# Kernel optimization log

Hardware: AMD Instinct MI355X
Metric: run time of the kernel (lower is better)

The kernel has to match this reference:

```python
import jax, jax.numpy as jnp
import numpy as np

# GNB per-element parameters [s, beta, R, C6] indexed by atomic number Z (rows not listed stay zero)
_ROWS = {
 1:[0.2772,1.7504,3.6516,95.99], 2:[0.2425,2.087,2.1843,40.67], 3:[0.3266,2.3073,1.2711,70.21],
 4:[0.3964,2.8811,3.3497,114.51], 5:[0.3121,2.6366,2.7079,152.36], 6:[0.2455,3.0189,1.8219,184.28],
 7:[0.2743,2.9432,2.4667,482.54], 8:[0.2577,2.7407,2.365,405.57], 9:[0.2791,2.5863,1.5062,218.45],
 10:[0.2378,2.5307,1.8233,174.81], 11:[0.2592,2.5679,1.3974,181.7], 12:[0.3837,2.9613,3.3515,263.02],
 13:[0.3013,3.2377,3.0102,228.1], 14:[0.3202,3.2749,3.1629,359.43], 15:[0.3399,3.7491,3.2554,3222.12],
 16:[0.3215,3.6718,2.9539,2144.49], 17:[0.3071,3.418,3.0368,2072.46], 18:[0.2752,3.3306,2.6598,1357.42],
 19:[0.2264,2.9736,4.0877,1406.65], 20:[0.4015,3.4464,4.1275,1058.36], 21:[0.9388,4.5955,9.7282,11498.73],
 22:[0.6048,3.5334,8.5322,3361.33], 23:[0.3678,3.068,7.2344,2095.91], 24:[0.2848,2.8393,5.3605,1049.31],
 25:[0.355,3.055,3.718,966.27], 26:[0.4406,3.2628,3.6408,1571.36], 27:[0.4124,3.2622,3.4961,1183.59],
 28:[0.3139,2.749,3.5108,787.76], 29:[0.3345,2.9097,3.0537,563.93], 30:[0.3391,2.9024,3.0261,592.91],
 31:[0.3146,3.3924,3.1735,430.82], 32:[0.3327,3.2804,3.1773,812.57], 33:[0.404,3.8757,3.8357,4533.53],
 34:[0.3343,3.8562,3.1109,3440.92], 35:[0.3242,3.7067,3.2122,3859.82], 36:[0.292,3.6457,2.8263,2729.6],
 37:[0.2677,3.4421,2.412,1864.19], 38:[0.3446,3.559,1.894,1175.73], 39:[1.0038,5.7293,11.2061,32141.18],
 40:[0.6146,5.075,6.821,27655.14], 41:[0.4244,3.7156,7.2367,2864.2], 42:[0.4882,3.6853,3.901,3563.45],
 43:[0.4439,3.6987,4.0857,3266.43], 44:[0.4736,3.7826,4.045,3967.23], 45:[0.4039,3.4706,3.4813,2233.82],
 46:[0.3188,3.3433,3.0487,1393.49], 47:[0.2948,3.1186,2.7795,1315.09], 48:[0.3012,3.0853,2.8673,1311.47],
 49:[0.3351,3.5452,3.3339,1460.56], 50:[0.3134,3.2997,3.0086,1662.99], 51:[0.4081,4.1277,3.9919,8089.97],
 52:[0.3585,4.1795,3.4209,6887.05], 53:[0.3574,4.0988,3.5649,8799.32], 54:[0.3134,4.0387,3.0288,6136.5],
 55:[0.2872,3.8468,2.262,3757.31], 56:[0.3788,4.0368,1.3837,2561.18], 57:[1.0851,6.1365,12.171,66580.83],
 72:[0.5577,5.213,6.0791,27593.76], 73:[0.5308,4.7637,5.7661,15364.65], 74:[0.3926,3.6018,3.6366,2734.5],
 75:[0.5351,3.9552,4.241,4801.82], 76:[0.4701,4.0278,4.1348,5685.94], 77:[0.3661,3.6123,3.4213,2786.0],
 78:[0.3411,3.6066,3.2486,2699.79], 79:[0.3164,3.3822,2.9588,2282.6], 80:[0.3047,3.375,2.9381,2476.79],
 81:[0.2802,3.3964,2.7711,2988.7], 82:[0.2682,3.2481,2.5816,2506.63], 83:[0.3876,4.1225,3.785,8916.84],
 84:[0.3679,4.2313,3.5381,8694.22], 85:[0.368,4.2455,3.6985,11821.61], 86:[0.3195,4.1784,3.0551,8410.64],
}
_TAB = np.zeros((87, 4), np.float32)
for _z, _v in _ROWS.items():
    _TAB[_z] = _v
GNB_TABLE = jnp.asarray(_TAB)
C_SP2 = jnp.asarray(np.array([0.2808, 3.0548, 2.2348, 429.69], np.float32))
C_SP3 = jnp.asarray(np.array([0.2455, 3.0189, 1.8219, 184.28], np.float32))
N_CN2 = jnp.asarray(np.array([0.2996, 3.02, 2.6454, 720.18], np.float32))
N_CN3 = jnp.asarray(np.array([0.2743, 2.9432, 2.4667, 482.54], np.float32))

BJ_A1, BJ_A2, BJ_ALPHA = 0.4, 4.0, 14.0
CUTOFF_LR, CUTOFF_START = 10.0, 8.0  # cutoff_start = cutoff_lr - 2.0


def _poly_envelope(x):
    # PolynomialCutoff.calculate_envelope with r_max=1, p=6:
    x6 = x ** 6
    env = 1.0 - 28.0 * x6 + 48.0 * x6 * x - 21.0 * x6 * x * x
    return env * (x < 1.0)


def _gnb_forward(lengths, Z, edge_index):
    n_nodes = Z.shape[0]
    sender, receiver = edge_index[0], edge_index[1]

    # coordination numbers via scatter-add on receiver
    cn = jnp.zeros((n_nodes,), jnp.int32).at[receiver].add(1)

    # species-indexed params with CN-adaptive selection for C and N
    params = GNB_TABLE[Z]  # [N, 4]
    c_params = jnp.where((cn <= 3)[:, None], C_SP2[None, :], C_SP3[None, :])
    n_params = jnp.where((cn <= 2)[:, None], N_CN2[None, :], N_CN3[None, :])
    params = jnp.where((Z == 6)[:, None], c_params, params)
    params = jnp.where((Z == 7)[:, None], n_params, params)

    R_i = params[:, 2]
    C6_i = params[:, 3]

    # geometric-mean combination rules per edge
    C6_ij = jnp.sqrt(C6_i[sender] * C6_i[receiver])
    R_ij = jnp.sqrt(R_i[sender] * R_i[receiver])

    r = lengths
    # BJ damping: f = 1 / (1 + 6 (r/r0)^(-alpha)), r0 = a1 sqrt(R_ij) + a2
    r0 = BJ_A1 * jnp.sqrt(R_ij) + BJ_A2
    f_damp = 1.0 / (1.0 + 6.0 * (r0 / r) ** BJ_ALPHA)

    e_edge = -C6_ij / (R_ij ** 6 + r ** 6) * f_damp

    # long-range polynomial cutoff switching from 1 at cutoff_start to 0 at cutoff_lr
    x = (r - CUTOFF_START) / (CUTOFF_LR - CUTOFF_START)
    env = jnp.where(r < CUTOFF_START, 1.0, _poly_envelope(x))
    e_edge = e_edge * env

    # scatter-sum to atoms; 0.5 to split symmetric pair energy over both directions
    node_energy = jnp.zeros((n_nodes,), e_edge.dtype).at[receiver].add(0.5 * e_edge)
    return node_energy


def setup_inputs() -> dict:
    key = jax.random.key(0)
    k1, k2, k3 = jax.random.split(key, 3)
    n_nodes, n_edges = 100000, 6400000
    Z = jax.random.randint(k1, (n_nodes,), 1, 87, dtype=jnp.int32)
    edge_index = jax.random.randint(k2, (2, n_edges), 0, n_nodes, dtype=jnp.int32)
    lengths = jax.random.uniform(k3, (n_edges,), jnp.float32, 1.0, 10.5)
    return {"Z": Z, "edge_index": edge_index, "lengths": lengths}


def reference(Z, edge_index, lengths):
    return _gnb_forward(lengths, Z, edge_index)
```

## Files before the change

kernel.cpp:

```cpp
#include <hip/hip_runtime.h>


#define B2SHIFT 10
#define B2SIZE  1024
#define TILE    4096
#define SBLK    512
#define NWAVE   8
#define ESLICES 32
#define MAXB    128
#define EB      256

__device__ __constant__ float2 GNB_RC6[87] = {
    {0.f, 0.f},
    {3.6516f, 95.99f},   {2.1843f, 40.67f},   {1.2711f, 70.21f},
    {3.3497f, 114.51f},  {2.7079f, 152.36f},  {1.8219f, 184.28f},
    {2.4667f, 482.54f},  {2.365f, 405.57f},   {1.5062f, 218.45f},
    {1.8233f, 174.81f},  {1.3974f, 181.7f},   {3.3515f, 263.02f},
    {3.0102f, 228.1f},   {3.1629f, 359.43f},  {3.2554f, 3222.12f},
    {2.9539f, 2144.49f}, {3.0368f, 2072.46f}, {2.6598f, 1357.42f},
    {4.0877f, 1406.65f}, {4.1275f, 1058.36f}, {9.7282f, 11498.73f},
    {8.5322f, 3361.33f}, {7.2344f, 2095.91f}, {5.3605f, 1049.31f},
    {3.718f, 966.27f},   {3.6408f, 1571.36f}, {3.4961f, 1183.59f},
    {3.5108f, 787.76f},  {3.0537f, 563.93f},  {3.0261f, 592.91f},
    {3.1735f, 430.82f},  {3.1773f, 812.57f},  {3.8357f, 4533.53f},
    {3.1109f, 3440.92f}, {3.2122f, 3859.82f}, {2.8263f, 2729.6f},
    {2.412f, 1864.19f},  {1.894f, 1175.73f},  {11.2061f, 32141.18f},
    {6.821f, 27655.14f}, {7.2367f, 2864.2f},  {3.901f, 3563.45f},
    {4.0857f, 3266.43f}, {4.045f, 3967.23f},  {3.4813f, 2233.82f},
    {3.0487f, 1393.49f}, {2.7795f, 1315.09f}, {2.8673f, 1311.47f},
    {3.3339f, 1460.56f}, {3.0086f, 1662.99f}, {3.9919f, 8089.97f},
    {3.4209f, 6887.05f}, {3.5649f, 8799.32f}, {3.0288f, 6136.5f},
    {2.262f, 3757.31f},  {1.3837f, 2561.18f}, {12.171f, 66580.83f},
    {0.f,0.f},{0.f,0.f},{0.f,0.f},{0.f,0.f},{0.f,0.f},{0.f,0.f},{0.f,0.f},
    {0.f,0.f},{0.f,0.f},{0.f,0.f},{0.f,0.f},{0.f,0.f},{0.f,0.f},{0.f,0.f},
    {6.0791f, 27593.76f}, {5.7661f, 15364.65f}, {3.6366f, 2734.5f},
    {4.241f, 4801.82f},   {4.1348f, 5685.94f},  {3.4213f, 2786.0f},
    {3.2486f, 2699.79f},  {2.9588f, 2282.6f},   {2.9381f, 2476.79f},
    {2.7711f, 2988.7f},   {2.5816f, 2506.63f},  {3.785f, 8916.84f},
    {3.5381f, 8694.22f},  {3.6985f, 11821.61f}, {3.0551f, 8410.64f},
};

__device__ __forceinline__ void atomic_fadd(float* p, float v) {
#if defined(__HIP_PLATFORM_AMD__)
    unsafeAtomicAdd(p, v);
#else
    atomicAdd(p, v);
#endif
}

__global__ void gnb_init(const int* __restrict__ Z, unsigned* __restrict__ isCN,
                         int nw, int n_nodes, int4* __restrict__ zp4, int zq,
                         int* __restrict__ zp, int zwords) {
    int stride = gridDim.x * blockDim.x;
    int t0 = blockIdx.x * blockDim.x + threadIdx.x;
    int4 z4 = make_int4(0, 0, 0, 0);
    for (int i = t0; i < zq; i += stride) zp4[i] = z4;
    for (int i = zq * 4 + t0; i < zwords; i += stride) zp[i] = 0;
    for (int w = t0; w < nw; w += stride) {
        unsigned m = 0;
        int base = w << 5;
        int lim = n_nodes - base; if (lim > 32) lim = 32;
        for (int k = 0; k < lim; ++k) {
            int z = Z[base + k];
            if (z == 6 || z == 7) m |= (1u << k);
        }
        isCN[w] = m;
    }
}

__global__ void __launch_bounds__(EB)
gnb_degree(const int* __restrict__ recv, const unsigned* __restrict__ isCN,
           int* __restrict__ cn, int n_edges) {
    int base = (blockIdx.x * EB + threadIdx.x) * 4;
    if (base + 3 < n_edges) {
        int4 rv = *(const int4*)(recv + base);
        int rr[4] = {rv.x, rv.y, rv.z, rv.w};
        #pragma unroll
        for (int j = 0; j < 4; ++j) {
            unsigned r = (unsigned)rr[j];
            if ((isCN[r >> 5] >> (r & 31)) & 1u) atomicAdd(&cn[r], 1);
        }
    } else {
        for (int j = 0; j < 4; ++j) {
            int e = base + j;
            if (e < n_edges) {
                unsigned r = (unsigned)recv[e];
                if ((isCN[r >> 5] >> (r & 31)) & 1u) atomicAdd(&cn[r], 1);
            }
        }
    }
}

__global__ void gnb_params(const int* __restrict__ Z, const int* __restrict__ cn,
                           float2* __restrict__ P2, int n_nodes) {
    int i = blockIdx.x * blockDim.x + threadIdx.x;
    if (i >= n_nodes) return;
    int z = Z[i];
    float Rp, C6;
    if (z == 6) {
        if (cn[i] <= 3) { Rp = 2.2348f; C6 = 429.69f; }
        else            { Rp = 1.8219f; C6 = 184.28f; }
    } else if (z == 7) {
        if (cn[i] <= 2) { Rp = 2.6454f; C6 = 720.18f; }
        else            { Rp = 2.4667f; C6 = 482.54f; }
    } else {
        float2 rc = GNB_RC6[z];
        Rp = rc.x; C6 = rc.y;
    }
    P2[i] = make_float2(sqrtf(C6), sqrtf(sqrtf(Rp)));
}

__device__ __forceinline__ float gnb_energy_eval(float2 ps, float2 pr, float rlen) {
    float env;
    if (rlen < 8.0f) {
        env = 1.0f;
    } else {
        float x = (rlen - 8.0f) * 0.5f;
        float x2 = x * x;
        float x6 = x2 * x2 * x2;
        env = 1.0f - 28.0f * x6 + 48.0f * x6 * x - 21.0f * x6 * x2;
    }
    float sR  = ps.y * pr.y;
    float C6  = ps.x * pr.x;
    float Rij = sR * sR;
    float R3  = Rij * Rij * Rij;
    float R6  = R3 * R3;
    float r0  = 0.4f * sR + 4.0f;
    float t   = r0 / rlen;
    float t2 = t * t, t4 = t2 * t2, t8 = t4 * t4;
    float t14 = t8 * t4 * t2;
    float fd = 1.0f / (1.0f + 6.0f * t14);
    float rl2 = rlen * rlen;
    float r6 = rl2 * rl2 * rl2;
    return -0.5f * C6 / (R6 + r6) * fd * env;
}

__global__ void __launch_bounds__(SBLK)
gnb_scatter(const int* __restrict__ send, const int* __restrict__ recv,
            const float* __restrict__ len, const float2* __restrict__ P2,
            uint2* __restrict__ buckets, unsigned* __restrict__ cursor,
            uint2* __restrict__ ovrec, unsigned* __restrict__ ocur,
            int n_edges, int cap, unsigned ocap, int NB2) {
    __shared__ unsigned hist[NWAVE][MAXB];
    __shared__ unsigned waveBase[NWAVE][MAXB];
    __shared__ unsigned cntS[MAXB];
    __shared__ unsigned startp[MAXB + 1];
    __shared__ unsigned gbase[MAXB];
    __shared__ uint2 srec[TILE];
    __shared__ unsigned char bmap[TILE];
    const int tid = threadIdx.x;
    const int w   = tid >> 6;
    const int e0  = blockIdx.x * TILE;

    for (int i = tid; i < NWAVE * MAXB; i += SBLK) (&hist[0][0])[i] = 0;
    __syncthreads();

    unsigned pk[2][4];
    float    ev[2][4];
    const bool full = (e0 + TILE <= n_edges);
    #pragma unroll
    for (int k = 0; k < 2; ++k) {
        int base = e0 + (k * SBLK + tid) * 4;
        int ss[4]; int rr[4]; float ll[4];
        if (full) {
            int4   sv = *(const int4*)(send + base);
            int4   rv = *(const int4*)(recv + base);
            float4 lv = *(const float4*)(len + base);
            ss[0]=sv.x; ss[1]=sv.y; ss[2]=sv.z; ss[3]=sv.w;
            rr[0]=rv.x; rr[1]=rv.y; rr[2]=rv.z; rr[3]=rv.w;
            ll[0]=lv.x; ll[1]=lv.y; ll[2]=lv.z; ll[3]=lv.w;
        } else {
            for (int j = 0; j < 4; ++j) {
                int e = base + j;
                bool ok = (e < n_edges);
                ss[j] = ok ? send[e] : 0;
                rr[j] = ok ? recv[e] : 0;
                ll[j] = ok ? len[e]  : 1.0e9f;
            }
        }
        #pragma unroll
        for (int j = 0; j < 4; ++j) {
            if (ll[j] < 10.0f) {
                float2 ps = P2[ss[j]];
                float2 pr = P2[rr[j]];
                ev[k][j] = gnb_energy_eval(ps, pr, ll[j]);
                unsigned r = (unsigned)rr[j];
                unsigned b = r >> B2SHIFT;
                unsigned off = atomicAdd(&hist[w][b], 1u);
                pk[k][j] = b | ((r & (B2SIZE - 1)) << 7) | (off << 17);
            } else {
                pk[k][j] = 0xFFFFFFFFu;
            }
        }
    }
    __syncthreads();

    if (tid < MAXB) {
        unsigned acc = 0;
        #pragma unroll
        for (int ww = 0; ww < NWAVE; ++ww) {
            waveBase[ww][tid] = acc;
            acc += hist[ww][tid];
        }
        cntS[tid] = acc;
    }
    __syncthreads();
    if (tid < 64) {
        unsigned a0 = cntS[2 * tid], a1 = cntS[2 * tid + 1];
        unsigned s = a0 + a1;
        unsigned sc = s;
        #pragma unroll
        for (int d = 1; d < 64; d <<= 1) {
            unsigned t = __shfl_up(sc, d);
            if (tid >= d) sc += t;
        }
        unsigned excl = sc - s;
        startp[2 * tid]     = excl;
        startp[2 * tid + 1] = excl + a0;
        if (tid == 63) startp[MAXB] = sc;
    }
    __syncthreads();
    if (tid < NB2) {
        unsigned c = cntS[tid];
        gbase[tid] = c ? atomicAdd(&cursor[tid], c) : 0u;
    }
    __syncthreads();

    #pragma unroll
    for (int k = 0; k < 2; ++k) {
        #pragma unroll
        for (int j = 0; j < 4; ++j) {
            unsigned p = pk[k][j];
            if (p != 0xFFFFFFFFu) {
                unsigned b    = p & (MAXB - 1);
                unsigned rlow = (p >> 7) & (B2SIZE - 1);
                unsigned off  = p >> 17;
                unsigned slot = startp[b] + waveBase[w][b] + off;
                srec[slot] = make_uint2(rlow, __float_as_uint(ev[k][j]));
                bmap[slot] = (unsigned char)b;
            }
        }
    }
    __syncthreads();

    unsigned total = startp[MAXB];
    for (unsigned i = tid; i < total; i += SBLK) {
        unsigned b = bmap[i];
        unsigned g = gbase[b] + (i - startp[b]);
        uint2 rec = srec[i];
        if (g < (unsigned)cap) {
            buckets[(size_t)b * cap + g] = rec;
        } else {
            unsigned o = atomicAdd(ocur, 1u);
            if (o < ocap) ovrec[o] = make_uint2((b << B2SHIFT) | rec.x, rec.y);
        }
    }
}

__global__ void __launch_bounds__(256)
gnb_accum(const uint2* __restrict__ buckets, const unsigned* __restrict__ cursor,
          float* __restrict__ rep, int cap) {
    __shared__ float acc[2][B2SIZE + 8];
    const int b   = blockIdx.x / ESLICES;
    const int sl  = blockIdx.x % ESLICES;
    const int tid = threadIdx.x;
    const int rr  = (tid >> 6) & 1;

    for (int i = tid; i < 2 * (B2SIZE + 8); i += 256) acc[0][i] = 0.0f;
    __syncthreads();

    unsigned count = cursor[b];
    if (count > (unsigned)cap) count = (unsigned)cap;
    unsigned seg = (count + ESLICES - 1) / ESLICES;
    unsigned st  = (unsigned)sl * seg;
    unsigned en  = st + seg; if (en > count) en = count;

    const uint2* src = buckets + (size_t)b * cap;
    for (unsigned i = st + tid; i < en; i += 256) {
        uint2 rec = src[i];
        atomicAdd(&acc[rr][rec.x], __uint_as_float(rec.y));
    }
    __syncthreads();

    float* dst = rep + (size_t)blockIdx.x * B2SIZE;
    for (int i = tid; i < B2SIZE; i += 256) dst[i] = acc[0][i] + acc[1][i];
}

__global__ void gnb_ovf_energy(const uint2* __restrict__ ovrec,
                               const unsigned* __restrict__ ocur,
                               float* __restrict__ ovf, unsigned ocap) {
    unsigned n = *ocur; if (n > ocap) n = ocap;
    int stride = gridDim.x * blockDim.x;
    for (unsigned i = blockIdx.x * blockDim.x + threadIdx.x; i < n; i += stride) {
        uint2 rec = ovrec[i];
        atomic_fadd(&ovf[rec.x], __uint_as_float(rec.y));
    }
}

__global__ void gnb_reduce(const float* __restrict__ rep, const float* __restrict__ ovf,
                           float* __restrict__ out, int n_nodes) {
    int i = blockIdx.x * blockDim.x + threadIdx.x;
    if (i >= n_nodes) return;
    int b = i >> B2SHIFT;
    int j = i & (B2SIZE - 1);
    const float* src = rep + ((size_t)b * ESLICES) * B2SIZE + j;
    float sum = ovf[i];
    #pragma unroll
    for (int s = 0; s < ESLICES; ++s) sum += src[(size_t)s * B2SIZE];
    out[i] = sum;
}

extern "C" void kernel_launch(void* const* d_in, const int* in_sizes, int n_in,
                              void* d_out, int out_size, void* d_ws, size_t ws_size,
                              hipStream_t stream) {
    const int*   Z    = (const int*)d_in[0];
    const int*   eidx = (const int*)d_in[1];
    const float* len  = (const float*)d_in[2];
    float*       out  = (float*)d_out;

    const int n_nodes = in_sizes[0];
    const int n_edges = in_sizes[2];
    const int* send = eidx;
    const int* recv = eidx + n_edges;

    const int NB2 = (n_nodes + B2SIZE - 1) >> B2SHIFT;
    const int nw  = (n_nodes + 31) >> 5;
    const int nwp = (nw + 7) & ~7;

    char* ws = (char*)d_ws;
    unsigned* cursor = (unsigned*)ws;
    unsigned* ocur   = (unsigned*)(ws + MAXB * 4);
    int*      cn     = (int*)(ws + (MAXB + 8) * 4);
    float*    ovf    = (float*)(ws + ((size_t)n_nodes + MAXB + 8) * 4);
    float2*   P2     = (float2*)(ws + ((size_t)2 * n_nodes + MAXB + 8) * 4);
    unsigned* isCN   = (unsigned*)(ws + ((size_t)4 * n_nodes + MAXB + 8) * 4);
    float*    rep    = (float*)((char*)isCN + (size_t)nwp * 4);
    size_t rep_w     = (size_t)NB2 * ESLICES * B2SIZE;
    char*     tail   = (char*)rep + rep_w * 4;

    size_t fixed_words = (size_t)4 * n_nodes + MAXB + 8 + nwp + rep_w;
    size_t total_words = ws_size / 4;
    size_t avail = total_words > fixed_words ? total_words - fixed_words : 0;
    size_t ovw = avail / 32;
    unsigned ocap = (unsigned)(ovw / 2);
    long cap = (long)((avail - ovw) / (2 * (size_t)NB2));
    if (cap > n_edges) cap = n_edges;
    if (cap < 0) cap = 0;
    uint2* ovrec   = (uint2*)tail;
    uint2* buckets = (uint2*)(tail + (size_t)ocap * 8);

    const int B = 256;
    int node_blocks = (n_nodes + B - 1) / B;
    int edge4_blocks = (n_edges + EB * 4 - 1) / (EB * 4);
    int scat_blocks = (n_edges + TILE - 1) / TILE;
    int zero_words  = 2 * n_nodes + MAXB + 8;
    int zq = zero_words / 4;

    gnb_init<<<256, B, 0, stream>>>(Z, isCN, nw, n_nodes, (int4*)ws, zq,
                                    (int*)ws, zero_words);
    gnb_degree<<<edge4_blocks, EB, 0, stream>>>(recv, isCN, cn, n_edges);
    gnb_params<<<node_blocks, B, 0, stream>>>(Z, cn, P2, n_nodes);
    gnb_scatter<<<scat_blocks, SBLK, 0, stream>>>(send, recv, len, P2, buckets,
                                                  cursor, ovrec, ocur, n_edges,
                                                  (int)cap, ocap, NB2);
    gnb_accum<<<NB2 * ESLICES, B, 0, stream>>>(buckets, cursor, rep, (int)cap);
    gnb_ovf_energy<<<8, B, 0, stream>>>(ovrec, ocur, ovf, ocap);
    gnb_reduce<<<node_blocks, B, 0, stream>>>(rep, ovf, out, n_nodes);
}
```

Before: 228.6 us.

## Write scatter records directly to global buckets and widen accum LDS replicas

The scatter kernel no longer stages records in shared memory sorted by bucket before writing them out. Each thread now computes its global slot from the bucket cursor base, the per-wave base and its offset, then writes the record straight to global memory. This drops the block-wide prefix scan, two barriers and about 36KB of LDS, which should raise occupancy, but the global stores become less coalesced. Separately, the accumulation kernel goes from 2 to 4 shared-memory accumulator replicas to reduce atomic contention, at the cost of more LDS to zero and a slightly larger final sum.

```diff
diff --git a/kernel.cpp b/kernel.cpp
--- a/kernel.cpp
+++ b/kernel.cpp
@@ -9,6 +9,7 @@
 #define ESLICES 32
 #define MAXB    128
 #define EB      256
+#define AREP    4
 
 __device__ __constant__ float2 GNB_RC6[87] = {
     {0.f, 0.f},
@@ -143,11 +144,7 @@
             int n_edges, int cap, unsigned ocap, int NB2) {
     __shared__ unsigned hist[NWAVE][MAXB];
     __shared__ unsigned waveBase[NWAVE][MAXB];
-    __shared__ unsigned cntS[MAXB];
-    __shared__ unsigned startp[MAXB + 1];
     __shared__ unsigned gbase[MAXB];
-    __shared__ uint2 srec[TILE];
-    __shared__ unsigned char bmap[TILE];
     const int tid = threadIdx.x;
     const int w   = tid >> 6;
     const int e0  = blockIdx.x * TILE;
@@ -202,27 +199,7 @@
             waveBase[ww][tid] = acc;
             acc += hist[ww][tid];
         }
-        cntS[tid] = acc;
-    }
-    __syncthreads();
-    if (tid < 64) {
-        unsigned a0 = cntS[2 * tid], a1 = cntS[2 * tid + 1];
-        unsigned s = a0 + a1;
-        unsigned sc = s;
-        #pragma unroll
-        for (int d = 1; d < 64; d <<= 1) {
-            unsigned t = __shfl_up(sc, d);
-            if (tid >= d) sc += t;
-        }
-        unsigned excl = sc - s;
-        startp[2 * tid]     = excl;
-        startp[2 * tid + 1] = excl + a0;
-        if (tid == 63) startp[MAXB] = sc;
-    }
-    __syncthreads();
-    if (tid < NB2) {
-        unsigned c = cntS[tid];
-        gbase[tid] = c ? atomicAdd(&cursor[tid], c) : 0u;
+        gbase[tid] = acc ? atomicAdd(&cursor[tid], acc) : 0u;
     }
     __syncthreads();
 
@@ -235,24 +212,15 @@
                 unsigned b    = p & (MAXB - 1);
                 unsigned rlow = (p >> 7) & (B2SIZE - 1);
                 unsigned off  = p >> 17;
-                unsigned slot = startp[b] + waveBase[w][b] + off;
-                srec[slot] = make_uint2(rlow, __float_as_uint(ev[k][j]));
-                bmap[slot] = (unsigned char)b;
+                unsigned g    = gbase[b] + waveBase[w][b] + off;
+                uint2 rec = make_uint2(rlow, __float_as_uint(ev[k][j]));
+                if (g < (unsigned)cap) {
+                    buckets[(size_t)b * cap + g] = rec;
+                } else {
+                    unsigned o = atomicAdd(ocur, 1u);
+                    if (o < ocap) ovrec[o] = make_uint2((b << B2SHIFT) | rlow, rec.y);
+                }
             }
-        }
-    }
-    __syncthreads();
-
-    unsigned total = startp[MAXB];
-    for (unsigned i = tid; i < total; i += SBLK) {
-        unsigned b = bmap[i];
-        unsigned g = gbase[b] + (i - startp[b]);
-        uint2 rec = srec[i];
-        if (g < (unsigned)cap) {
-            buckets[(size_t)b * cap + g] = rec;
-        } else {
-            unsigned o = atomicAdd(ocur, 1u);
-            if (o < ocap) ovrec[o] = make_uint2((b << B2SHIFT) | rec.x, rec.y);
         }
     }
 }
@@ -260,13 +228,13 @@
 __global__ void __launch_bounds__(256)
 gnb_accum(const uint2* __restrict__ buckets, const unsigned* __restrict__ cursor,
           float* __restrict__ rep, int cap) {
-    __shared__ float acc[2][B2SIZE + 8];
+    __shared__ float acc[AREP][B2SIZE + 8];
     const int b   = blockIdx.x / ESLICES;
     const int sl  = blockIdx.x % ESLICES;
     const int tid = threadIdx.x;
-    const int rr  = (tid >> 6) & 1;
-
-    for (int i = tid; i < 2 * (B2SIZE + 8); i += 256) acc[0][i] = 0.0f;
+    const int rr  = (tid >> 6) & (AREP - 1);
+
+    for (int i = tid; i < AREP * (B2SIZE + 8); i += 256) acc[0][i] = 0.0f;
     __syncthreads();
 
     unsigned count = cursor[b];
@@ -283,7 +251,8 @@
     __syncthreads();
 
     float* dst = rep + (size_t)blockIdx.x * B2SIZE;
-    for (int i = tid; i < B2SIZE; i += 256) dst[i] = acc[0][i] + acc[1][i];
+    for (int i = tid; i < B2SIZE; i += 256)
+        dst[i] = (acc[0][i] + acc[1][i]) + (acc[2][i] + acc[3][i]);
 }
 
 __global__ void gnb_ovf_energy(const uint2* __restrict__ ovrec,
```

After: 237.8 us. +4.1%, slower.
